# Optimization experiments

Measured on AMD Instinct MI355X. Metric: run time of the kernel, lower is better.

Reference implementation:

```python
import jax, jax.numpy as jnp
import numpy as np

N_NODES = 100000
N_EDGES = 1600000
IN_FEATS = 128
N_HIDDEN = 128
N_CLASSES = 64


def setup_inputs() -> dict:
    key = jax.random.key(0)
    ks = jax.random.split(key, 8)
    def glorot(k, shape):
        fan_in, fan_out = shape
        lim = (6.0 / (fan_in + fan_out)) ** 0.5
        return jax.random.uniform(k, shape, jnp.float32, -lim, lim)
    return {
        "x": jax.random.normal(ks[0], (N_NODES, IN_FEATS), jnp.float32),
        "W_self1": glorot(ks[1], (IN_FEATS, N_HIDDEN)),
        "W_neigh1": glorot(ks[2], (IN_FEATS, N_HIDDEN)),
        "b1": jnp.zeros((N_HIDDEN,), jnp.float32),
        "W_self2": glorot(ks[3], (N_HIDDEN, N_HIDDEN)),
        "W_neigh2": glorot(ks[4], (N_HIDDEN, N_HIDDEN)),
        "b2": jnp.zeros((N_HIDDEN,), jnp.float32),
        "W_out": glorot(ks[5], (N_HIDDEN, N_CLASSES)),
        "b_out": jnp.zeros((N_CLASSES,), jnp.float32),
        "edge_src": jax.random.randint(ks[6], (N_EDGES,), 0, N_NODES, jnp.int32),
        "edge_dst": jax.random.randint(ks[7], (N_EDGES,), 0, N_NODES, jnp.int32),
    }


def reference(x, W_self1, W_neigh1, b1, W_self2, W_neigh2, b2, W_out, b_out,
              edge_src, edge_dst):
    n = x.shape[0]
    # in-degree for mean aggregation (clamped to 1 to avoid div-by-zero)
    deg = jax.ops.segment_sum(jnp.ones_like(edge_dst, jnp.float32), edge_dst,
                              num_segments=n)
    inv_deg = 1.0 / jnp.maximum(deg, 1.0)  # [N]

    def sage_conv(h, W_self, W_neigh, b):
        # mean aggregation: gather src features, scatter-sum to dst, divide by degree
        msg_sum = jax.ops.segment_sum(h[edge_src], edge_dst, num_segments=n)
        h_neigh = msg_sum * inv_deg[:, None]            # [N, d]
        return h @ W_self + h_neigh @ W_neigh + b       # fc_self + fc_neigh + bias

    # layer 0 + relu (dropout is identity in eval mode)
    h = jax.nn.relu(sage_conv(x, W_self1, W_neigh1, b1))
    # layer 1 + relu
    h = jax.nn.relu(sage_conv(h, W_self2, W_neigh2, b2))
    # final linear classifier
    return h @ W_out + b_out
```

## Files before the change

### kernel.cpp

```cpp
#include <hip/hip_runtime.h>
#include <hip/hip_bf16.h>


#define N_FEATS 128
#define CAP 64
#define TILE 4096

typedef __attribute__((ext_vector_type(8))) short bf16x8;
typedef __attribute__((ext_vector_type(4))) float f32x4;
typedef __attribute__((ext_vector_type(2))) float f32x2;

__device__ __forceinline__ ushort f2b(float f) {
    union { float f; unsigned u; } c; c.f = f;
    unsigned u = c.u + 0x7fffu + ((c.u >> 16) & 1u);
    return (ushort)(u >> 16);
}
__device__ __forceinline__ float u2f(unsigned u) {
    union { unsigned u; float f; } c; c.u = u;
    return c.f;
}

__device__ __forceinline__ void scan512(const int* __restrict__ gsrc,
                                        int* sA, int* sB, int t) {
    sA[t] = gsrc[t];
    sA[t + 256] = gsrc[t + 256];
    __syncthreads();
    int* src = sA;
    int* dst = sB;
    for (int off = 1; off < 512; off <<= 1) {
#pragma unroll
        for (int i = t; i < 512; i += 256) {
            int v = src[i];
            if (i >= off) v += src[i - off];
            dst[i] = v;
        }
        __syncthreads();
        int* tmp = src; src = dst; dst = tmp;
    }
    if (src != sA) {
        sA[t] = src[t];
        sA[t + 256] = src[t + 256];
        __syncthreads();
    }
}

__global__ __launch_bounds__(256) void k_histprep(
    const int* __restrict__ dst, int* __restrict__ bucketCnt, int E, int NT,
    const float* __restrict__ x, ushort* __restrict__ xb, int n4,
    const float* __restrict__ Ws1, const float* __restrict__ Wn1,
    const float* __restrict__ Ws2, const float* __restrict__ Wn2,
    const float* __restrict__ Wo,
    ushort* __restrict__ o1, ushort* __restrict__ o2,
    ushort* __restrict__ o3, ushort* __restrict__ o4,
    ushort* __restrict__ o5, ushort* __restrict__ hzrow, int N) {
    __shared__ int h[512];
    int t = threadIdx.x;
    if (blockIdx.x < NT) {
        h[t] = 0; h[t + 256] = 0;
        __syncthreads();
        int base0 = blockIdx.x * TILE;
#pragma unroll
        for (int j = 0; j < 16; ++j) {
            int i = base0 + j * 256 + t;
            if (i < E) atomicAdd(&h[dst[i] >> 8], 1);
        }
        __syncthreads();
        for (int b = t; b < 512; b += 256)
            if (h[b] > 0) atomicAdd(&bucketCnt[b], h[b]);
    } else {
        int i = (blockIdx.x - NT) * 256 + t;
        if (i < n4) {
            float4 v = ((const float4*)x)[i];
            ushort4 o;
            o.x = f2b(v.x); o.y = f2b(v.y); o.z = f2b(v.z); o.w = f2b(v.w);
            ((ushort4*)xb)[i] = o;
        } else {
            int q = i - n4;
            if (q < 65536) {
                int w = q >> 14, j = q & 16383;
                const float* W = (w == 0) ? Ws1 : (w == 1) ? Wn1 : (w == 2) ? Ws2 : Wn2;
                ushort* O = (w == 0) ? o1 : (w == 1) ? o2 : (w == 2) ? o3 : o4;
                int k = j >> 7, n = j & 127;
                O[n * 128 + k] = f2b(W[j]);
            } else if (q < 65536 + 8192) {
                int j = q - 65536;
                int k = j >> 6, n = j & 63;
                o5[n * 128 + k] = f2b(Wo[j]);
            } else if (q < 65536 + 8192 + 64) {
                int j = q - (65536 + 8192);
                ushort4 z = {0, 0, 0, 0};
                if (j < 32) ((ushort4*)&xb[(size_t)N * N_FEATS])[j] = z;
                else        ((ushort4*)hzrow)[j - 32] = z;
            }
        }
    }
}

__global__ __launch_bounds__(256) void k_scatter(const int* __restrict__ src,
                                                 const int* __restrict__ dst,
                                                 const int* __restrict__ bucketCnt,
                                                 int* __restrict__ cursor0,
                                                 int* __restrict__ ebuf, int E) {
    __shared__ int th[512];
    __shared__ int sA[512];
    __shared__ int sB[512];
    int t = threadIdx.x;
    th[t] = 0; th[t + 256] = 0;
    __syncthreads();
    int base0 = blockIdx.x * TILE;
    int pk[16], bk[16], rk[16];
#pragma unroll
    for (int j = 0; j < 16; ++j) {
        int i = base0 + j * 256 + t;
        bk[j] = -1;
        if (i < E) {
            int d = dst[i], s = src[i];
            bk[j] = d >> 8;
            pk[j] = ((d & 255) << 17) | s;
            rk[j] = atomicAdd(&th[bk[j]], 1);
        }
    }
    __syncthreads();
    scan512(bucketCnt, sA, sB, t);
    for (int b = t; b < 512; b += 256) {
        int c = th[b];
        if (c > 0) {
            int base_b = sA[b] - bucketCnt[b];
            th[b] = base_b + atomicAdd(&cursor0[b], c);
        }
    }
    __syncthreads();
#pragma unroll
    for (int j = 0; j < 16; ++j)
        if (bk[j] >= 0) ebuf[th[bk[j]] + rk[j]] = pk[j];
}

__global__ __launch_bounds__(256) void k_csr(const int* __restrict__ bucketCnt,
                                             const int* __restrict__ ebuf,
                                             int* __restrict__ cnt,
                                             int* __restrict__ colF, int N) {
    __shared__ int cl[256];
    __shared__ int sA[512];
    __shared__ int sB[512];
    int t = threadIdx.x, b = blockIdx.x;
    cl[t] = 0;
    __syncthreads();
    scan512(bucketCnt, sA, sB, t);
    int hi = sA[b];
    int lo = hi - bucketCnt[b];
    int node0 = b << 8;
    for (int i = lo + t; i < hi; i += 256) {
        int p = ebuf[i];
        int s = p & 0x1FFFF;
        int dl = p >> 17;
        int r = atomicAdd(&cl[dl], 1);
        if (r < CAP) colF[((size_t)(node0 + dl)) * CAP + r] = s;
    }
    __syncthreads();
    int n = node0 + t;
    if (n < N) cnt[n] = cl[t];
}

__global__ __launch_bounds__(256) void k_agg(const ushort* __restrict__ h,
                                             const int* __restrict__ cnt,
                                             const int* __restrict__ colF,
                                             ushort* __restrict__ hn, int N) {
    int n = blockIdx.x * 4 + (threadIdx.x >> 6);
    if (n >= N) return;
    int lane = threadIdx.x & 63;
    int g = lane >> 4;
    int f = lane & 15;
    int degT = cnt[n];
    int deg = degT > CAP ? CAP : degT;
    const int* __restrict__ row = &colF[(size_t)n * CAP];
    f32x2 acc[4];
#pragma unroll
    for (int k = 0; k < 4; ++k) acc[k] = (f32x2){0.f, 0.f};

    for (int j0 = 0; j0 < deg; j0 += 16) {
        int last = deg - 1;
        int ja = j0 + g, jb = j0 + 4 + g, jc = j0 + 8 + g, jd = j0 + 12 + g;
        int sa = __builtin_nontemporal_load(&row[min(ja, last)]);
        int sb = __builtin_nontemporal_load(&row[min(jb, last)]);
        int sc = __builtin_nontemporal_load(&row[min(jc, last)]);
        int sd = __builtin_nontemporal_load(&row[min(jd, last)]);
        sa = (ja < deg) ? sa : N;
        sb = (jb < deg) ? sb : N;
        sc = (jc < deg) ? sc : N;
        sd = (jd < deg) ? sd : N;
        uint4 va = *(const uint4*)&h[(size_t)sa * N_FEATS + f * 8];
        uint4 vb = *(const uint4*)&h[(size_t)sb * N_FEATS + f * 8];
        uint4 vc = *(const uint4*)&h[(size_t)sc * N_FEATS + f * 8];
        uint4 vd = *(const uint4*)&h[(size_t)sd * N_FEATS + f * 8];
        unsigned wa[4] = {va.x, va.y, va.z, va.w};
        unsigned wb[4] = {vb.x, vb.y, vb.z, vb.w};
        unsigned wc[4] = {vc.x, vc.y, vc.z, vc.w};
        unsigned wd[4] = {vd.x, vd.y, vd.z, vd.w};
#pragma unroll
        for (int k = 0; k < 4; ++k) {
            acc[k] += (f32x2){u2f(wa[k] << 16), u2f(wa[k] & 0xffff0000u)};
            acc[k] += (f32x2){u2f(wb[k] << 16), u2f(wb[k] & 0xffff0000u)};
            acc[k] += (f32x2){u2f(wc[k] << 16), u2f(wc[k] & 0xffff0000u)};
            acc[k] += (f32x2){u2f(wd[k] << 16), u2f(wd[k] & 0xffff0000u)};
        }
    }
#pragma unroll
    for (int k = 0; k < 4; ++k) {
        acc[k].x += __shfl_xor(acc[k].x, 16, 64);
        acc[k].y += __shfl_xor(acc[k].y, 16, 64);
        acc[k].x += __shfl_xor(acc[k].x, 32, 64);
        acc[k].y += __shfl_xor(acc[k].y, 32, 64);
    }
    if (g == 0) {
        float inv = 1.f / fmaxf((float)degT, 1.f);
        uint4 o;
        unsigned ow[4];
#pragma unroll
        for (int k = 0; k < 4; ++k) {
            unsigned lo = f2b(acc[k].x * inv);
            unsigned hi = f2b(acc[k].y * inv);
            ow[k] = lo | (hi << 16);
        }
        o.x = ow[0]; o.y = ow[1]; o.z = ow[2]; o.w = ow[3];
        *(uint4*)&hn[(size_t)n * N_FEATS + f * 8] = o;
    }
}

__global__ __launch_bounds__(256) void k_mm1(const ushort* __restrict__ A1,
                                             const ushort* __restrict__ Wst,
                                             const ushort* __restrict__ HN,
                                             const ushort* __restrict__ Wnt,
                                             const float* __restrict__ bias,
                                             ushort* __restrict__ Hout, int M) {
    constexpr int LDA = 40;
    __shared__ ushort As[128 * LDA];
    __shared__ ushort Bs[128 * LDA];
    const int t = threadIdx.x;
    const int w = t >> 6, lane = t & 63;
    const int l15 = lane & 15, quad = lane >> 4;
    const int wr = (w >> 1) * 64, wc = (w & 1) * 64;
    const int row0 = blockIdx.x * 128;

    f32x4 acc[4][4];
#pragma unroll
    for (int mi = 0; mi < 4; ++mi)
#pragma unroll
        for (int ni = 0; ni < 4; ++ni) acc[mi][ni] = (f32x4){0.f, 0.f, 0.f, 0.f};

    for (int kt = 0; kt < 8; ++kt) {
        const ushort* __restrict__ A = (kt < 4) ? A1 : HN;
        const ushort* __restrict__ W = (kt < 4) ? Wst : Wnt;
        const int k0 = (kt & 3) * 32;
        __syncthreads();
#pragma unroll
        for (int i = 0; i < 2; ++i) {
            int slot = t + i * 256;
            int r = slot >> 2, ko = (slot & 3) * 8;
            int row = row0 + r;
            if (row >= M) row = M - 1;
            *(bf16x8*)&As[r * LDA + ko] = *(const bf16x8*)&A[(size_t)row * N_FEATS + k0 + ko];
            *(bf16x8*)&Bs[r * LDA + ko] = *(const bf16x8*)&W[(size_t)r * N_FEATS + k0 + ko];
        }
        __syncthreads();
        bf16x8 af[4];
#pragma unroll
        for (int mi = 0; mi < 4; ++mi)
            af[mi] = *(const bf16x8*)&As[(wr + mi * 16 + l15) * LDA + quad * 8];
#pragma unroll
        for (int ni = 0; ni < 4; ++ni) {
            bf16x8 bfr = *(const bf16x8*)&Bs[(wc + ni * 16 + l15) * LDA + quad * 8];
#pragma unroll
            for (int mi = 0; mi < 4; ++mi)
                acc[mi][ni] = __builtin_amdgcn_mfma_f32_16x16x32_bf16(
                    af[mi], bfr, acc[mi][ni], 0, 0, 0);
        }
    }
#pragma unroll
    for (int ni = 0; ni < 4; ++ni) {
        int c = wc + ni * 16 + l15;
        float bv = bias[c];
#pragma unroll
        for (int mi = 0; mi < 4; ++mi)
#pragma unroll
            for (int r = 0; r < 4; ++r) {
                int row = row0 + wr + mi * 16 + quad * 4 + r;
                if (row < M)
                    Hout[(size_t)row * N_FEATS + c] = f2b(fmaxf(acc[mi][ni][r] + bv, 0.f));
            }
    }
}

__global__ __launch_bounds__(256) void k_mm2cls(const ushort* __restrict__ A1,
                                                const ushort* __restrict__ Wst,
                                                const ushort* __restrict__ HN,
                                                const ushort* __restrict__ Wnt,
                                                const float* __restrict__ bias,
                                                const ushort* __restrict__ Wot,
                                                const float* __restrict__ bout,
                                                float* __restrict__ OutF, int M) {
    constexpr int LDA = 40;
    __shared__ ushort As[128 * LDA];
    __shared__ ushort Bs[128 * LDA];
    const int t = threadIdx.x;
    const int w = t >> 6, lane = t & 63;
    const int l15 = lane & 15, quad = lane >> 4;
    const int wr = (w >> 1) * 64, wc = (w & 1) * 64;
    const int row0 = blockIdx.x * 128;

    f32x4 acc[4][4];
#pragma unroll
    for (int mi = 0; mi < 4; ++mi)
#pragma unroll
        for (int ni = 0; ni < 4; ++ni) acc[mi][ni] = (f32x4){0.f, 0.f, 0.f, 0.f};

    for (int kt = 0; kt < 8; ++kt) {
        const ushort* __restrict__ A = (kt < 4) ? A1 : HN;
        const ushort* __restrict__ W = (kt < 4) ? Wst : Wnt;
        const int k0 = (kt & 3) * 32;
        __syncthreads();
#pragma unroll
        for (int i = 0; i < 2; ++i) {
            int slot = t + i * 256;
            int r = slot >> 2, ko = (slot & 3) * 8;
            int row = row0 + r;
            if (row >= M) row = M - 1;
            *(bf16x8*)&As[r * LDA + ko] = *(const bf16x8*)&A[(size_t)row * N_FEATS + k0 + ko];
            *(bf16x8*)&Bs[r * LDA + ko] = *(const bf16x8*)&W[(size_t)r * N_FEATS + k0 + ko];
        }
        __syncthreads();
        bf16x8 af[4];
#pragma unroll
        for (int mi = 0; mi < 4; ++mi)
            af[mi] = *(const bf16x8*)&As[(wr + mi * 16 + l15) * LDA + quad * 8];
#pragma unroll
        for (int ni = 0; ni < 4; ++ni) {
            bf16x8 bfr = *(const bf16x8*)&Bs[(wc + ni * 16 + l15) * LDA + quad * 8];
#pragma unroll
            for (int mi = 0; mi < 4; ++mi)
                acc[mi][ni] = __builtin_amdgcn_mfma_f32_16x16x32_bf16(
                    af[mi], bfr, acc[mi][ni], 0, 0, 0);
        }
    }

    f32x4 acc2[2][4];
#pragma unroll
    for (int mi = 0; mi < 2; ++mi)
#pragma unroll
        for (int ni = 0; ni < 4; ++ni) acc2[mi][ni] = (f32x4){0.f, 0.f, 0.f, 0.f};

    for (int kt = 0; kt < 4; ++kt) {
        const int k0 = kt * 32;
        __syncthreads();
        {
            int r = t >> 2, ko = (t & 3) * 8;
            if (r < 64)
                *(bf16x8*)&Bs[r * LDA + ko] =
                    *(const bf16x8*)&Wot[(size_t)r * N_FEATS + k0 + ko];
        }
        if ((w & 1) == (k0 >> 6)) {
            int ni0 = (k0 & 63) >> 4;
#pragma unroll
            for (int d = 0; d < 2; ++d) {
                int ni = ni0 + d;
                int c = wc + ni * 16 + l15;
                int cc = c - k0;
                float bv = bias[c];
#pragma unroll
                for (int mi = 0; mi < 4; ++mi)
#pragma unroll
                    for (int r = 0; r < 4; ++r) {
                        int lrow = wr + mi * 16 + quad * 4 + r;
                        As[lrow * LDA + cc] = f2b(fmaxf(acc[mi][ni][r] + bv, 0.f));
                    }
            }
        }
        __syncthreads();
        bf16x8 af2[2];
#pragma unroll
        for (int mi = 0; mi < 2; ++mi)
            af2[mi] = *(const bf16x8*)&As[(w * 32 + mi * 16 + l15) * LDA + quad * 8];
#pragma unroll
        for (int ni = 0; ni < 4; ++ni) {
            bf16x8 bfr = *(const bf16x8*)&Bs[(ni * 16 + l15) * LDA + quad * 8];
#pragma unroll
            for (int mi = 0; mi < 2; ++mi)
                acc2[mi][ni] = __builtin_amdgcn_mfma_f32_16x16x32_bf16(
                    af2[mi], bfr, acc2[mi][ni], 0, 0, 0);
        }
    }
#pragma unroll
    for (int ni = 0; ni < 4; ++ni) {
        int c = ni * 16 + l15;
        float bv = bout[c];
#pragma unroll
        for (int mi = 0; mi < 2; ++mi)
#pragma unroll
            for (int r = 0; r < 4; ++r) {
                int row = row0 + w * 32 + mi * 16 + quad * 4 + r;
                if (row < M)
                    OutF[(size_t)row * 64 + c] = acc2[mi][ni][r] + bv;
            }
    }
}

extern "C" void kernel_launch(void* const* d_in, const int* in_sizes, int n_in,
                              void* d_out, int out_size, void* d_ws, size_t ws_size,
                              hipStream_t stream) {
    const float* x        = (const float*)d_in[0];
    const float* W_self1  = (const float*)d_in[1];
    const float* W_neigh1 = (const float*)d_in[2];
    const float* b1       = (const float*)d_in[3];
    const float* W_self2  = (const float*)d_in[4];
    const float* W_neigh2 = (const float*)d_in[5];
    const float* b2       = (const float*)d_in[6];
    const float* W_out    = (const float*)d_in[7];
    const float* b_out    = (const float*)d_in[8];
    const int* edge_src   = (const int*)d_in[9];
    const int* edge_dst   = (const int*)d_in[10];

    const int N = in_sizes[0] / N_FEATS;
    const int E = in_sizes[9];
    float* out = (float*)d_out;

    char* ws = (char*)d_ws;
    size_t o = 0;
    auto carve = [&](size_t bytes) -> char* {
        char* p = ws + o;
        o += (bytes + 255) & ~(size_t)255;
        return p;
    };
    ushort* xb    = (ushort*)carve((size_t)(N + 1) * N_FEATS * 2);
    ushort* h     = (ushort*)carve((size_t)(N + 1) * N_FEATS * 2);
    ushort* hn    = (ushort*)carve((size_t)N * N_FEATS * 2);
    int* colF     = (int*)carve((size_t)N * CAP * 4);
    int* cnt      = (int*)carve((size_t)N * 4);
    int* ebuf     = (int*)carve((size_t)E * 4);
    int* bwork    = (int*)carve(1024 * 4);
    ushort* Ws1t  = (ushort*)carve(128 * 128 * 2);
    ushort* Wn1t  = (ushort*)carve(128 * 128 * 2);
    ushort* Ws2t  = (ushort*)carve(128 * 128 * 2);
    ushort* Wn2t  = (ushort*)carve(128 * 128 * 2);
    ushort* Wot   = (ushort*)carve(64 * 128 * 2);
    (void)ws_size;
    int* bucketCnt = bwork;
    int* cursor0   = bwork + 512;

    const int NB = (N + 255) >> 8;
    const int NT = (E + TILE - 1) / TILE;
    const int n4 = N * N_FEATS / 4;
    const int PREP = n4 + 65536 + 8192 + 64;
    const int PREP_B = (PREP + 255) / 256;

    hipMemsetAsync(bwork, 0, 1024 * 4, stream);
    k_histprep<<<NT + PREP_B, 256, 0, stream>>>(
        edge_dst, bucketCnt, E, NT,
        x, xb, n4, W_self1, W_neigh1, W_self2, W_neigh2, W_out,
        Ws1t, Wn1t, Ws2t, Wn2t, Wot, &h[(size_t)N * N_FEATS], N);
    k_scatter<<<NT, 256, 0, stream>>>(edge_src, edge_dst, bucketCnt, cursor0, ebuf, E);
    k_csr<<<NB, 256, 0, stream>>>(bucketCnt, ebuf, cnt, colF, N);

    const int GB = (N + 127) / 128;
    const int AB = (N + 3) / 4;

    k_agg<<<AB, 256, 0, stream>>>(xb, cnt, colF, hn, N);
    k_mm1<<<GB, 256, 0, stream>>>(xb, Ws1t, hn, Wn1t, b1, h, N);
    k_agg<<<AB, 256, 0, stream>>>(h, cnt, colF, hn, N);
    k_mm2cls<<<GB, 256, 0, stream>>>(h, Ws2t, hn, Wn2t, b2, Wot, b_out, out, N);
}
```

Before: 341.6 us.

## Aggregate layer-1 neighbors from an FP8 copy of x; widen GEMM K tiles with swizzle

The prep kernel now also writes an FP8 (e4m3) copy of the input features. The first aggregation gathers 16-byte FP8 rows per lane for nodes with degree 8 or more, halving gather bytes, and keeps the bf16 path for low-degree nodes. Separately, both GEMM kernels load 64-wide K tiles with an XOR-swizzled LDS layout, which halves the number of barrier phases and is meant to reduce bank conflicts. The FP8 gather loses precision in the layer-1 neighbor mean, which risks exceeding tolerance, and it adds an extra write of x during prep.

After: 362.7 us. 1.06x slower.

```diff
diff --git a/kernel.cpp b/kernel.cpp
--- a/kernel.cpp
+++ b/kernel.cpp
@@ -46,7 +46,8 @@
 
 __global__ __launch_bounds__(256) void k_histprep(
     const int* __restrict__ dst, int* __restrict__ bucketCnt, int E, int NT,
-    const float* __restrict__ x, ushort* __restrict__ xb, int n4,
+    const float* __restrict__ x, ushort* __restrict__ xb,
+    unsigned char* __restrict__ xq, int n4,
     const float* __restrict__ Ws1, const float* __restrict__ Wn1,
     const float* __restrict__ Ws2, const float* __restrict__ Wn2,
     const float* __restrict__ Wo,
@@ -74,6 +75,9 @@
             ushort4 o;
             o.x = f2b(v.x); o.y = f2b(v.y); o.z = f2b(v.z); o.w = f2b(v.w);
             ((ushort4*)xb)[i] = o;
+            int w8 = __builtin_amdgcn_cvt_pk_fp8_f32(v.x, v.y, 0, false);
+            w8 = __builtin_amdgcn_cvt_pk_fp8_f32(v.z, v.w, w8, true);
+            ((unsigned*)xq)[i] = (unsigned)w8;
         } else {
             int q = i - n4;
             if (q < 65536) {
@@ -86,11 +90,11 @@
                 int j = q - 65536;
                 int k = j >> 6, n = j & 63;
                 o5[n * 128 + k] = f2b(Wo[j]);
-            } else if (q < 65536 + 8192 + 64) {
+            } else if (q < 65536 + 8192 + 96) {
                 int j = q - (65536 + 8192);
-                ushort4 z = {0, 0, 0, 0};
-                if (j < 32) ((ushort4*)&xb[(size_t)N * N_FEATS])[j] = z;
-                else        ((ushort4*)hzrow)[j - 32] = z;
+                if (j < 32) { ushort4 z = {0,0,0,0}; ((ushort4*)&xb[(size_t)N * N_FEATS])[j] = z; }
+                else if (j < 64) { ushort4 z = {0,0,0,0}; ((ushort4*)hzrow)[j - 32] = z; }
+                else ((unsigned*)&xq[(size_t)N * N_FEATS])[j - 64] = 0u;
             }
         }
     }
@@ -161,6 +165,116 @@
     if (n < N) cnt[n] = cl[t];
 }
 
+__global__ __launch_bounds__(256) void k_agg8(const unsigned char* __restrict__ xq,
+                                              const ushort* __restrict__ hb,
+                                              const int* __restrict__ cnt,
+                                              const int* __restrict__ colF,
+                                              ushort* __restrict__ hn, int N) {
+    int n = blockIdx.x * 4 + (threadIdx.x >> 6);
+    if (n >= N) return;
+    int lane = threadIdx.x & 63;
+    int degT = cnt[n];
+    int deg = degT > CAP ? CAP : degT;
+    const int* __restrict__ row = &colF[(size_t)n * CAP];
+    float inv = 1.f / fmaxf((float)degT, 1.f);
+
+    if (deg >= 8) {
+        int g = lane >> 3, f = lane & 7;
+        f32x2 acc[8];
+#pragma unroll
+        for (int k = 0; k < 8; ++k) acc[k] = (f32x2){0.f, 0.f};
+        for (int j0 = 0; j0 < deg; j0 += 32) {
+            int last = deg - 1;
+            int jj[4], ss[4];
+#pragma unroll
+            for (int q = 0; q < 4; ++q) {
+                jj[q] = j0 + q * 8 + g;
+                ss[q] = __builtin_nontemporal_load(&row[min(jj[q], last)]);
+                ss[q] = (jj[q] < deg) ? ss[q] : N;
+            }
+            uint4 v[4];
+#pragma unroll
+            for (int q = 0; q < 4; ++q)
+                v[q] = *(const uint4*)&xq[(size_t)ss[q] * N_FEATS + f * 16];
+#pragma unroll
+            for (int q = 0; q < 4; ++q) {
+                unsigned wd[4] = {v[q].x, v[q].y, v[q].z, v[q].w};
+#pragma unroll
+                for (int d = 0; d < 4; ++d) {
+                    acc[2 * d]     += __builtin_amdgcn_cvt_pk_f32_fp8((int)wd[d], false);
+                    acc[2 * d + 1] += __builtin_amdgcn_cvt_pk_f32_fp8((int)wd[d], true);
+                }
+            }
+        }
+#pragma unroll
+        for (int k = 0; k < 8; ++k) {
+            acc[k].x += __shfl_xor(acc[k].x, 8, 64);
+            acc[k].y += __shfl_xor(acc[k].y, 8, 64);
+            acc[k].x += __shfl_xor(acc[k].x, 16, 64);
+            acc[k].y += __shfl_xor(acc[k].y, 16, 64);
+            acc[k].x += __shfl_xor(acc[k].x, 32, 64);
+            acc[k].y += __shfl_xor(acc[k].y, 32, 64);
+        }
+        if (g == 0) {
+            unsigned ow[8];
+#pragma unroll
+            for (int j = 0; j < 8; ++j)
+                ow[j] = (unsigned)f2b(acc[j].x * inv) | ((unsigned)f2b(acc[j].y * inv) << 16);
+            uint4 o0 = {ow[0], ow[1], ow[2], ow[3]};
+            uint4 o1 = {ow[4], ow[5], ow[6], ow[7]};
+            *(uint4*)&hn[(size_t)n * N_FEATS + f * 16] = o0;
+            *(uint4*)&hn[(size_t)n * N_FEATS + f * 16 + 8] = o1;
+        }
+    } else {
+        int g = lane >> 4, f = lane & 15;
+        f32x2 acc[4];
+#pragma unroll
+        for (int k = 0; k < 4; ++k) acc[k] = (f32x2){0.f, 0.f};
+        for (int j0 = 0; j0 < deg; j0 += 16) {
+            int last = deg - 1;
+            int ja = j0 + g, jb = j0 + 4 + g, jc = j0 + 8 + g, jd = j0 + 12 + g;
+            int sa = __builtin_nontemporal_load(&row[min(ja, last)]);
+            int sb = __builtin_nontemporal_load(&row[min(jb, last)]);
+            int sc = __builtin_nontemporal_load(&row[min(jc, last)]);
+            int sd = __builtin_nontemporal_load(&row[min(jd, last)]);
+            sa = (ja < deg) ? sa : N;
+            sb = (jb < deg) ? sb : N;
+            sc = (jc < deg) ? sc : N;
+            sd = (jd < deg) ? sd : N;
+            uint4 va = *(const uint4*)&hb[(size_t)sa * N_FEATS + f * 8];
+            uint4 vb = *(const uint4*)&hb[(size_t)sb * N_FEATS + f * 8];
+            uint4 vc = *(const uint4*)&hb[(size_t)sc * N_FEATS + f * 8];
+            uint4 vd = *(const uint4*)&hb[(size_t)sd * N_FEATS + f * 8];
+            unsigned wa[4] = {va.x, va.y, va.z, va.w};
+            unsigned wb[4] = {vb.x, vb.y, vb.z, vb.w};
+            unsigned wc2[4] = {vc.x, vc.y, vc.z, vc.w};
+            unsigned wd2[4] = {vd.x, vd.y, vd.z, vd.w};
+#pragma unroll
+            for (int k = 0; k < 4; ++k) {
+                acc[k] += (f32x2){u2f(wa[k] << 16), u2f(wa[k] & 0xffff0000u)};
+                acc[k] += (f32x2){u2f(wb[k] << 16), u2f(wb[k] & 0xffff0000u)};
+                acc[k] += (f32x2){u2f(wc2[k] << 16), u2f(wc2[k] & 0xffff0000u)};
+                acc[k] += (f32x2){u2f(wd2[k] << 16), u2f(wd2[k] & 0xffff0000u)};
+            }
+        }
+#pragma unroll
+        for (int k = 0; k < 4; ++k) {
+            acc[k].x += __shfl_xor(acc[k].x, 16, 64);
+            acc[k].y += __shfl_xor(acc[k].y, 16, 64);
+            acc[k].x += __shfl_xor(acc[k].x, 32, 64);
+            acc[k].y += __shfl_xor(acc[k].y, 32, 64);
+        }
+        if (g == 0) {
+            unsigned ow[4];
+#pragma unroll
+            for (int k = 0; k < 4; ++k)
+                ow[k] = (unsigned)f2b(acc[k].x * inv) | ((unsigned)f2b(acc[k].y * inv) << 16);
+            uint4 o = {ow[0], ow[1], ow[2], ow[3]};
+            *(uint4*)&hn[(size_t)n * N_FEATS + f * 8] = o;
+        }
+    }
+}
+
 __global__ __launch_bounds__(256) void k_agg(const ushort* __restrict__ h,
                                              const int* __restrict__ cnt,
                                              const int* __restrict__ colF,
@@ -213,15 +327,11 @@
     }
     if (g == 0) {
         float inv = 1.f / fmaxf((float)degT, 1.f);
-        uint4 o;
         unsigned ow[4];
 #pragma unroll
-        for (int k = 0; k < 4; ++k) {
-            unsigned lo = f2b(acc[k].x * inv);
-            unsigned hi = f2b(acc[k].y * inv);
-            ow[k] = lo | (hi << 16);
-        }
-        o.x = ow[0]; o.y = ow[1]; o.z = ow[2]; o.w = ow[3];
+        for (int k = 0; k < 4; ++k)
+            ow[k] = (unsigned)f2b(acc[k].x * inv) | ((unsigned)f2b(acc[k].y * inv) << 16);
+        uint4 o = {ow[0], ow[1], ow[2], ow[3]};
         *(uint4*)&hn[(size_t)n * N_FEATS + f * 8] = o;
     }
 }
@@ -232,9 +342,9 @@
                                              const ushort* __restrict__ Wnt,
                                              const float* __restrict__ bias,
                                              ushort* __restrict__ Hout, int M) {
-    constexpr int LDA = 40;
-    __shared__ ushort As[128 * LDA];
-    __shared__ ushort Bs[128 * LDA];
+    constexpr int LDB = 72;
+    __shared__ ushort As[128 * LDB];
+    __shared__ ushort Bs[128 * LDB];
     const int t = threadIdx.x;
     const int w = t >> 6, lane = t & 63;
     const int l15 = lane & 15, quad = lane >> 4;
@@ -247,32 +357,39 @@
 #pragma unroll
         for (int ni = 0; ni < 4; ++ni) acc[mi][ni] = (f32x4){0.f, 0.f, 0.f, 0.f};
 
-    for (int kt = 0; kt < 8; ++kt) {
-        const ushort* __restrict__ A = (kt < 4) ? A1 : HN;
-        const ushort* __restrict__ W = (kt < 4) ? Wst : Wnt;
-        const int k0 = (kt & 3) * 32;
-        __syncthreads();
-#pragma unroll
-        for (int i = 0; i < 2; ++i) {
-            int slot = t + i * 256;
-            int r = slot >> 2, ko = (slot & 3) * 8;
+    for (int ph = 0; ph < 4; ++ph) {
+        const ushort* __restrict__ A = (ph < 2) ? A1 : HN;
+        const ushort* __restrict__ W = (ph < 2) ? Wst : Wnt;
+        const int k0 = (ph & 1) * 64;
+        __syncthreads();
+#pragma unroll
+        for (int i = 0; i < 4; ++i) {
+            int s = t + i * 256;
+            int r = s >> 3, ko = (s & 7) * 8;
+            int kos = ko ^ ((r & 3) * 8);
             int row = row0 + r;
             if (row >= M) row = M - 1;
-            *(bf16x8*)&As[r * LDA + ko] = *(const bf16x8*)&A[(size_t)row * N_FEATS + k0 + ko];
-            *(bf16x8*)&Bs[r * LDA + ko] = *(const bf16x8*)&W[(size_t)r * N_FEATS + k0 + ko];
-        }
-        __syncthreads();
-        bf16x8 af[4];
-#pragma unroll
-        for (int mi = 0; mi < 4; ++mi)
-            af[mi] = *(const bf16x8*)&As[(wr + mi * 16 + l15) * LDA + quad * 8];
-#pragma unroll
-        for (int ni = 0; ni < 4; ++ni) {
-            bf16x8 bfr = *(const bf16x8*)&Bs[(wc + ni * 16 + l15) * LDA + quad * 8];
-#pragma unroll
-            for (int mi = 0; mi < 4; ++mi)
-                acc[mi][ni] = __builtin_amdgcn_mfma_f32_16x16x32_bf16(
-                    af[mi], bfr, acc[mi][ni], 0, 0, 0);
+            *(bf16x8*)&As[r * LDB + kos] = *(const bf16x8*)&A[(size_t)row * N_FEATS + k0 + ko];
+            *(bf16x8*)&Bs[r * LDB + kos] = *(const bf16x8*)&W[(size_t)r * N_FEATS + k0 + ko];
+        }
+        __syncthreads();
+#pragma unroll
+        for (int sub = 0; sub < 2; ++sub) {
+            bf16x8 af[4];
+#pragma unroll
+            for (int mi = 0; mi < 4; ++mi) {
+                int R = wr + mi * 16 + l15;
+                af[mi] = *(const bf16x8*)&As[R * LDB + (sub * 32 + ((quad ^ (R & 3)) * 8))];
+            }
+#pragma unroll
+            for (int ni = 0; ni < 4; ++ni) {
+                int R2 = wc + ni * 16 + l15;
+                bf16x8 bfr = *(const bf16x8*)&Bs[R2 * LDB + (sub * 32 + ((quad ^ (R2 & 3)) * 8))];
+#pragma unroll
+                for (int mi = 0; mi < 4; ++mi)
+                    acc[mi][ni] = __builtin_amdgcn_mfma_f32_16x16x32_bf16(
+                        af[mi], bfr, acc[mi][ni], 0, 0, 0);
+            }
         }
     }
 #pragma unroll
@@ -298,9 +415,9 @@
                                                 const ushort* __restrict__ Wot,
                                                 const float* __restrict__ bout,
                                                 float* __restrict__ OutF, int M) {
-    constexpr int LDA = 40;
-    __shared__ ushort As[128 * LDA];
-    __shared__ ushort Bs[128 * LDA];
+    constexpr int LDB = 72;
+    __shared__ ushort As[128 * LDB];
+    __shared__ ushort Bs[128 * LDB];
     const int t = threadIdx.x;
     const int w = t >> 6, lane = t & 63;
     const int l15 = lane & 15, quad = lane >> 4;
@@ -313,32 +430,39 @@
 #pragma unroll
         for (int ni = 0; ni < 4; ++ni) acc[mi][ni] = (f32x4){0.f, 0.f, 0.f, 0.f};
 
-    for (int kt = 0; kt < 8; ++kt) {
-        const ushort* __restrict__ A = (kt < 4) ? A1 : HN;
-        const ushort* __restrict__ W = (kt < 4) ? Wst : Wnt;
-        const int k0 = (kt & 3) * 32;
-        __syncthreads();
-#pragma unroll
-        for (int i = 0; i < 2; ++i) {
-            int slot = t + i * 256;
-            int r = slot >> 2, ko = (slot & 3) * 8;
+    for (int ph = 0; ph < 4; ++ph) {
+        const ushort* __restrict__ A = (ph < 2) ? A1 : HN;
+        const ushort* __restrict__ W = (ph < 2) ? Wst : Wnt;
+        const int k0 = (ph & 1) * 64;
+        __syncthreads();
+#pragma unroll
+        for (int i = 0; i < 4; ++i) {
+            int s = t + i * 256;
+            int r = s >> 3, ko = (s & 7) * 8;
+            int kos = ko ^ ((r & 3) * 8);
             int row = row0 + r;
             if (row >= M) row = M - 1;
-            *(bf16x8*)&As[r * LDA + ko] = *(const bf16x8*)&A[(size_t)row * N_FEATS + k0 + ko];
-            *(bf16x8*)&Bs[r * LDA + ko] = *(const bf16x8*)&W[(size_t)r * N_FEATS + k0 + ko];
-        }
-        __syncthreads();
-        bf16x8 af[4];
-#pragma unroll
-        for (int mi = 0; mi < 4; ++mi)
-            af[mi] = *(const bf16x8*)&As[(wr + mi * 16 + l15) * LDA + quad * 8];
-#pragma unroll
-        for (int ni = 0; ni < 4; ++ni) {
-            bf16x8 bfr = *(const bf16x8*)&Bs[(wc + ni * 16 + l15) * LDA + quad * 8];
-#pragma unroll
-            for (int mi = 0; mi < 4; ++mi)
-                acc[mi][ni] = __builtin_amdgcn_mfma_f32_16x16x32_bf16(
-                    af[mi], bfr, acc[mi][ni], 0, 0, 0);
+            *(bf16x8*)&As[r * LDB + kos] = *(const bf16x8*)&A[(size_t)row * N_FEATS + k0 + ko];
+            *(bf16x8*)&Bs[r * LDB + kos] = *(const bf16x8*)&W[(size_t)r * N_FEATS + k0 + ko];
+        }
+        __syncthreads();
+#pragma unroll
+        for (int sub = 0; sub < 2; ++sub) {
+            bf16x8 af[4];
+#pragma unroll
+            for (int mi = 0; mi < 4; ++mi) {
+                int R = wr + mi * 16 + l15;
+                af[mi] = *(const bf16x8*)&As[R * LDB + (sub * 32 + ((quad ^ (R & 3)) * 8))];
+            }
+#pragma unroll
+            for (int ni = 0; ni < 4; ++ni) {
+                int R2 = wc + ni * 16 + l15;
+                bf16x8 bfr = *(const bf16x8*)&Bs[R2 * LDB + (sub * 32 + ((quad ^ (R2 & 3)) * 8))];
+#pragma unroll
+                for (int mi = 0; mi < 4; ++mi)
+                    acc[mi][ni] = __builtin_amdgcn_mfma_f32_16x16x32_bf16(
+                        af[mi], bfr, acc[mi][ni], 0, 0, 0);
+            }
         }
     }
 
@@ -354,7 +478,7 @@
         {
             int r = t >> 2, ko = (t & 3) * 8;
             if (r < 64)
-                *(bf16x8*)&Bs[r * LDA + ko] =
+                *(bf16x8*)&Bs[r * LDB + ko] =
                     *(const bf16x8*)&Wot[(size_t)r * N_FEATS + k0 + ko];
         }
         if ((w & 1) == (k0 >> 6)) {
@@ -370,7 +494,7 @@
 #pragma unroll
                     for (int r = 0; r < 4; ++r) {
                         int lrow = wr + mi * 16 + quad * 4 + r;
-                        As[lrow * LDA + cc] = f2b(fmaxf(acc[mi][ni][r] + bv, 0.f));
+                        As[lrow * LDB + cc] = f2b(fmaxf(acc[mi][ni][r] + bv, 0.f));
                     }
             }
         }
@@ -378,10 +502,10 @@
         bf16x8 af2[2];
 #pragma unroll
         for (int mi = 0; mi < 2; ++mi)
-            af2[mi] = *(const bf16x8*)&As[(w * 32 + mi * 16 + l15) * LDA + quad * 8];
+            af2[mi] = *(const bf16x8*)&As[(w * 32 + mi * 16 + l15) * LDB + quad * 8];
 #pragma unroll
         for (int ni = 0; ni < 4; ++ni) {
-            bf16x8 bfr = *(const bf16x8*)&Bs[(ni * 16 + l15) * LDA + quad * 8];
+            bf16x8 bfr = *(const bf16x8*)&Bs[(ni * 16 + l15) * LDB + quad * 8];
 #pragma unroll
             for (int mi = 0; mi < 2; ++mi)
                 acc2[mi][ni] = __builtin_amdgcn_mfma_f32_16x16x32_bf16(
@@ -432,6 +556,7 @@
     ushort* xb    = (ushort*)carve((size_t)(N + 1) * N_FEATS * 2);
     ushort* h     = (ushort*)carve((size_t)(N + 1) * N_FEATS * 2);
     ushort* hn    = (ushort*)carve((size_t)N * N_FEATS * 2);
+    unsigned char* xq = (unsigned char*)carve((size_t)(N + 1) * N_FEATS);
     int* colF     = (int*)carve((size_t)N * CAP * 4);
     int* cnt      = (int*)carve((size_t)N * 4);
     int* ebuf     = (int*)carve((size_t)E * 4);
@@ -448,13 +573,13 @@
     const int NB = (N + 255) >> 8;
     const int NT = (E + TILE - 1) / TILE;
     const int n4 = N * N_FEATS / 4;
-    const int PREP = n4 + 65536 + 8192 + 64;
+    const int PREP = n4 + 65536 + 8192 + 96;
     const int PREP_B = (PREP + 255) / 256;
 
     hipMemsetAsync(bwork, 0, 1024 * 4, stream);
     k_histprep<<<NT + PREP_B, 256, 0, stream>>>(
         edge_dst, bucketCnt, E, NT,
-        x, xb, n4, W_self1, W_neigh1, W_self2, W_neigh2, W_out,
+        x, xb, xq, n4, W_self1, W_neigh1, W_self2, W_neigh2, W_out,
         Ws1t, Wn1t, Ws2t, Wn2t, Wot, &h[(size_t)N * N_FEATS], N);
     k_scatter<<<NT, 256, 0, stream>>>(edge_src, edge_dst, bucketCnt, cursor0, ebuf, E);
     k_csr<<<NB, 256, 0, stream>>>(bucketCnt, ebuf, cnt, colF, N);
@@ -462,7 +587,7 @@
     const int GB = (N + 127) / 128;
     const int AB = (N + 3) / 4;
 
-    k_agg<<<AB, 256, 0, stream>>>(xb, cnt, colF, hn, N);
+    k_agg8<<<AB, 256, 0, stream>>>(xq, xb, cnt, colF, hn, N);
     k_mm1<<<GB, 256, 0, stream>>>(xb, Ws1t, hn, Wn1t, b1, h, N);
     k_agg<<<AB, 256, 0, stream>>>(h, cnt, colF, hn, N);
     k_mm2cls<<<GB, 256, 0, stream>>>(h, Ws2t, hn, Wn2t, b2, Wot, b_out, out, N);
```
